# Optimization experiments

Hardware: AMD Instinct MI355X
Metric: run time of the kernel (lower is better)

## Reference

```python
import jax, jax.numpy as jnp
import numpy as np
from jax import lax

K = 9  # propagation kernel

def conv(x, w, b, pad):
    y = lax.conv_general_dilated(x, w, (1, 1), [(pad, pad), (pad, pad)],
                                 dimension_numbers=('NCHW', 'OIHW', 'NCHW'))
    return y + b[None, :, None, None]

def bn(x, g, beta):
    # SynchronizedBatchNorm2d in eval mode with identity running stats (mean=0, var=1)
    return x * g[None, :, None, None] + beta[None, :, None, None]

def propagate(deep, wts):
    # Dynamic local filtering (same math as img2col * weights, sum over 81 taps),
    # computed as 81 shifted-slice FMAs instead of materializing the (n,c,hw,81) tensor.
    p = K // 2
    n, c, h, w = deep.shape
    padded = jnp.pad(deep, ((0, 0), (0, 0), (p, p), (p, p)))
    out = jnp.zeros_like(deep)
    for k in range(K * K):  # k = dy*9 + dx, matching unfold(2).unfold(3) flattening
        dy, dx = k // K, k % K
        out = out + padded[:, :, dy:dy + h, dx:dx + w] * wts[:, k:k + 1]
    return out

def setup_inputs():
    key = jax.random.key(0)
    ks = jax.random.split(key, 40)
    N, C, H, W = 1, 256, 96, 192
    NUM_CLASSES = 19
    s = 0.05
    f32 = jnp.float32
    d = {}
    d['f1_deep'] = jax.random.normal(ks[0], (N, C, H, W), f32)
    d['f1_low'] = jax.random.normal(ks[1], (N, C, H, W), f32)
    d['f2_low'] = jax.random.normal(ks[2], (N, C, H, W), f32)
    # WeightPredictor
    d['wp_c1_w'] = jax.random.normal(ks[3], (256, 256, 3, 3), f32) * s
    d['wp_c1_b'] = jnp.zeros((256,), f32)
    d['wp_c2_w'] = jax.random.normal(ks[4], (256, 512, 3, 3), f32) * s
    d['wp_c2_b'] = jnp.zeros((256,), f32)
    d['wp_fc_w'] = jax.random.normal(ks[5], (81, 256, 1, 1), f32) * s
    d['wp_fc_b'] = jnp.zeros((81,), f32)
    # AdaptiveScheduler
    d['sch_c1_w'] = jax.random.normal(ks[6], (256, 256, 3, 3), f32) * s
    d['sch_c1_b'] = jnp.zeros((256,), f32)
    d['sch_c2_w'] = jax.random.normal(ks[7], (256, 256, 3, 3), f32) * s
    d['sch_c2_b'] = jnp.zeros((256,), f32)
    d['sch_fc_w'] = jax.random.normal(ks[8], (1, 256), f32) * s
    d['sch_fc_b'] = jnp.zeros((1,), f32)
    # AdaptNet
    d['ad_c1_w'] = jax.random.normal(ks[9], (256, 512, 3, 3), f32) * s
    d['ad_c1_b'] = jnp.zeros((256,), f32)
    d['ad_c2_w'] = jax.random.normal(ks[10], (256, 256, 3, 3), f32) * s
    d['ad_c2_b'] = jnp.zeros((256,), f32)
    d['ad_c3_w'] = jax.random.normal(ks[11], (256, 256, 3, 3), f32) * s
    d['ad_c3_b'] = jnp.zeros((256,), f32)
    # reduce_conv2 (1x1 conv + BN)
    d['rc_w'] = jax.random.normal(ks[12], (48, 256, 1, 1), f32) * s
    d['rc_b'] = jnp.zeros((48,), f32)
    d['rc_g'] = jnp.ones((48,), f32)
    d['rc_beta'] = jnp.zeros((48,), f32)
    # last_conv
    d['lc1_w'] = jax.random.normal(ks[13], (256, 304, 3, 3), f32) * s
    d['lc1_b'] = jnp.zeros((256,), f32)
    d['lc1_g'] = jnp.ones((256,), f32)
    d['lc1_beta'] = jnp.zeros((256,), f32)
    d['lc2_w'] = jax.random.normal(ks[14], (256, 256, 3, 3), f32) * s
    d['lc2_b'] = jnp.zeros((256,), f32)
    d['lc2_g'] = jnp.ones((256,), f32)
    d['lc2_beta'] = jnp.zeros((256,), f32)
    d['lc3_w'] = jax.random.normal(ks[15], (NUM_CLASSES, 256, 1, 1), f32) * s
    d['lc3_b'] = jnp.zeros((NUM_CLASSES,), f32)
    return d

def reference(f1_deep, f1_low, f2_low,
              wp_c1_w, wp_c1_b, wp_c2_w, wp_c2_b, wp_fc_w, wp_fc_b,
              sch_c1_w, sch_c1_b, sch_c2_w, sch_c2_b, sch_fc_w, sch_fc_b,
              ad_c1_w, ad_c1_b, ad_c2_w, ad_c2_b, ad_c3_w, ad_c3_b,
              rc_w, rc_b, rc_g, rc_beta,
              lc1_w, lc1_b, lc1_g, lc1_beta,
              lc2_w, lc2_b, lc2_g, lc2_beta,
              lc3_w, lc3_b):
    n, c, h, w = f1_deep.shape
    # WeightPredictor: shared conv1 applied to both low features, cat, conv2, 1x1, softmax over 81 taps
    a1 = conv(f1_low, wp_c1_w, wp_c1_b, 1)
    a2 = conv(f2_low, wp_c1_w, wp_c1_b, 1)
    f = conv(jnp.concatenate([a1, a2], axis=1), wp_c2_w, wp_c2_b, 1)
    kernel = jax.nn.softmax(conv(f, wp_fc_w, wp_fc_b, 0), axis=1)  # (n,81,h,w)
    # AdaptiveScheduler
    diff = conv(f1_low, sch_c1_w, sch_c1_b, 1) - conv(f2_low, sch_c1_w, sch_c1_b, 1)
    o = conv(diff, sch_c2_w, sch_c2_b, 1)
    pooled = jnp.mean(o, axis=(2, 3)).squeeze()  # (256,) since n=1
    deviation = pooled @ sch_fc_w.T + sch_fc_b  # (1,)
    # PropagationModule (dynamic 9x9 local filtering of f1_deep by predicted per-pixel kernel)
    prop = propagate(f1_deep, kernel)  # (n,256,h,w)
    # AdaptNet
    x = conv(jnp.concatenate([f2_low, prop], axis=1), ad_c1_w, ad_c1_b, 1)
    x = conv(x, ad_c2_w, ad_c2_b, 1)
    x = conv(x, ad_c3_w, ad_c3_b, 1)
    # reduce_conv2 + last_conv
    low = bn(conv(f2_low, rc_w, rc_b, 0), rc_g, rc_beta)  # (n,48,h,w)
    x = jnp.concatenate([x, low], axis=1)  # (n,304,h,w)
    x = bn(conv(x, lc1_w, lc1_b, 1), lc1_g, lc1_beta)
    x = bn(conv(x, lc2_w, lc2_b, 1), lc2_g, lc2_beta)
    x = conv(x, lc3_w, lc3_b, 0)  # (n,19,h,w)
    out = jax.image.resize(x, (x.shape[0], x.shape[1], 4 * h, 4 * w), method='bilinear')
    return (out, deviation)
```

## Files before the change

### kernel.cpp

```cpp
#include <hip/hip_runtime.h>
#include <math.h>

#define HWIMG 18432
#define W2 194
#define H2 98
#define NPX1 (H2 * W2)
#define W4 200
#define H4 104
#define NPX4 (H4 * W4)
#define NOUT (19 * 384 * 768)

typedef short bf16x8 __attribute__((ext_vector_type(8)));
typedef float f32x16 __attribute__((ext_vector_type(16)));

__device__ __forceinline__ ushort bf16r(float f) {
    union { float f; unsigned u; } a; a.f = f;
    unsigned u = a.u;
    return (ushort)((u + 0x7fffu + ((u >> 16) & 1u)) >> 16);
}
__device__ __forceinline__ float b2f(ushort u) {
    union { unsigned i; float f; } a; a.i = ((unsigned)u) << 16;
    return a.f;
}
__device__ __forceinline__ bf16x8 ld8(const ushort* p) {
    return *reinterpret_cast<const bf16x8*>(p);
}

__device__ __forceinline__ void gld16(const ushort* g, ushort* l) {
    __builtin_amdgcn_global_load_lds(
        (const __attribute__((address_space(1))) unsigned int*)g,
        (__attribute__((address_space(3))) unsigned int*)l, 16, 0, 0);
}

#define MF(a, b, c) __builtin_amdgcn_mfma_f32_32x32x16_bf16(a, b, c, 0, 0, 0)

__device__ __forceinline__ int swz(int L) { return L ^ (((L >> 7) & 7) << 4); }


__global__ __launch_bounds__(256) void xform_t_k(const float* __restrict__ src,
                                                 const float* __restrict__ src2,
                                                 ushort* __restrict__ dst)
{
    const int px = blockIdx.x * 32 + (threadIdx.x & 31);
    const int c8 = (blockIdx.y * 8 + (threadIdx.x >> 5)) * 8;
    if (px >= NPX1) return;
    const int yP = px / W2, xP = px % W2;
    const int y = yP - 1, x = xP - 1;
    ushort v[8];
    if (y >= 0 && y < 96 && x >= 0 && x < 192) {
        const int p = y * 192 + x;
#pragma unroll
        for (int j = 0; j < 8; ++j) {
            float f = src[(size_t)(c8 + j) * HWIMG + p];
            if (src2) f -= src2[(size_t)(c8 + j) * HWIMG + p];
            v[j] = bf16r(f);
        }
    } else {
#pragma unroll
        for (int j = 0; j < 8; ++j) v[j] = 0;
    }
    *reinterpret_cast<uint4*>(dst + ((size_t)(c8 >> 4) * NPX1 + px) * 16 + (c8 & 15))
        = *reinterpret_cast<uint4*>(v);
}

__global__ __launch_bounds__(256) void xform_nhwc_k(const float* __restrict__ src,
                                                    ushort* __restrict__ dst)
{
    const int px = blockIdx.x * 8 + (threadIdx.x >> 5);
    const int c8 = (threadIdx.x & 31) * 8;
    if (px >= NPX4) return;
    const int yP = px / W4, xP = px % W4;
    const int y = yP - 4, x = xP - 4;
    ushort v[8];
    if (y >= 0 && y < 96 && x >= 0 && x < 192) {
        const int p = y * 192 + x;
#pragma unroll
        for (int j = 0; j < 8; ++j) v[j] = bf16r(src[(size_t)(c8 + j) * HWIMG + p]);
    } else {
#pragma unroll
        for (int j = 0; j < 8; ++j) v[j] = 0;
    }
    *reinterpret_cast<uint4*>(dst + (size_t)px * 256 + c8) = *reinterpret_cast<uint4*>(v);
}

__global__ __launch_bounds__(256) void borderzero3_k(ushort* __restrict__ b0,
                                                     ushort* __restrict__ b1,
                                                     ushort* __restrict__ b2)
{
    ushort* buf = (blockIdx.y == 0) ? b0 : ((blockIdx.y == 1) ? b1 : b2);
    const int idx = blockIdx.x * 256 + threadIdx.x;
    if (idx >= 580 * 16) return;
    const int pi = idx % 580;
    const int cb = idx / 580;
    int pp;
    if (pi < 194) pp = pi;
    else if (pi < 388) pp = 97 * 194 + (pi - 194);
    else if (pi < 484) pp = (pi - 388 + 1) * 194;
    else pp = (pi - 484 + 1) * 194 + 193;
    uint4 z = {0, 0, 0, 0};
    ushort* p = buf + ((size_t)cb * NPX1 + pp) * 16;
    *reinterpret_cast<uint4*>(p) = z;
    *reinterpret_cast<uint4*>(p + 8) = z;
}

struct WtxJob {
    const float* w; const float* b; const float* g; const float* beta;
    int CoutR, Coutp, CinR0, kb0e, CinR1, KBt, ntaps, wtoff, biasoff;
};

__global__ __launch_bounds__(256) void wtx_multi_k(WtxJob J0, WtxJob J1, WtxJob J2,
                                                   WtxJob J3, WtxJob J4, WtxJob J5,
                                                   ushort* __restrict__ wt,
                                                   float* __restrict__ biasout)
{
    WtxJob J = J0;
    switch (blockIdx.y) {
        case 1: J = J1; break; case 2: J = J2; break; case 3: J = J3; break;
        case 4: J = J4; break; case 5: J = J5; break; default: break;
    }
    const int idx = blockIdx.x * 256 + threadIdx.x;
    const int total = J.ntaps * J.KBt * J.Coutp * 16;
    const int CinT = J.CinR0 + J.CinR1;
    if (idx < total) {
        const int c16 = idx & 15;
        const int oc = (idx >> 4) % J.Coutp;
        const int r2 = idx / (16 * J.Coutp);
        const int tap = r2 % J.ntaps;
        const int kbt = r2 / J.ntaps;
        const int k = kbt * 16 + c16;
        float val = 0.f;
        if (oc < J.CoutR) {
            int cit = -1;
            if (k < J.kb0e) { if (k < J.CinR0) cit = k; }
            else { const int k1 = k - J.kb0e; if (k1 < J.CinR1) cit = J.CinR0 + k1; }
            if (cit >= 0) {
                val = J.w[((size_t)oc * CinT + cit) * J.ntaps + tap];
                if (J.g) val *= J.g[oc];
            }
        }
        wt[J.wtoff + idx] = bf16r(val);
    } else if (idx < total + J.Coutp) {
        const int oc = idx - total;
        float v = 0.f;
        if (oc < J.CoutR) {
            v = J.b ? J.b[oc] : 0.f;
            if (J.g) v = v * J.g[oc] + J.beta[oc];
        }
        biasout[J.biasoff + oc] = v;
    }
}

struct ConvJob {
    const ushort* in0; const ushort* in1;
    int KB0, KB1;
    const ushort* wt;
    const float* bias;
    ushort* out;
    int CoutWr;
};

template<int NTAPS>
__global__ __launch_bounds__(128) void conv_lds_k(ConvJob j0, ConvJob j1, ConvJob j2,
                                                  int Coutp)
{
    constexpr int AROWS = (NTAPS == 9) ? 4 : 2;
    constexpr int AW = (NTAPS == 9) ? 66 : 64;
    constexpr int ASLOTS = AROWS * AW * 2;
    __shared__ __align__(128) ushort Abuf[AROWS * AW * 16];
    __shared__ __align__(128) ushort Bbuf[NTAPS * 64 * 16];

    ConvJob J = j0;
    if (blockIdx.y == 1) J = j1;
    else if (blockIdx.y == 2) J = j2;

    const int nblk = gridDim.x;
    const int cpx = nblk >> 3;
    const int sw = ((int)blockIdx.x & 7) * cpx + ((int)blockIdx.x >> 3);
    const int pt = sw % 144;
    const int ocb0 = (sw / 144) * 64;
    const int y0 = (pt / 3) * 2 + 1;
    const int x0 = (pt % 3) * 64 + 1;

    const int tid = threadIdx.x;
    const int lane = tid & 63;
    const int wm = tid >> 6;
    const int l31 = lane & 31;
    const int h16 = (lane >> 5) * 16;

    const int bl = swz(tid * 16);
    const int b_r = bl >> 5;
    const int b_h8 = ((bl >> 4) & 1) * 8;

    const int KBtot = J.KB0 + J.KB1;

    f32x16 c00 = {}, c01 = {}, c10 = {}, c11 = {};

    for (int kb = 0; kb < KBtot; ++kb) {
        const ushort* plane = (kb < J.KB0)
            ? (J.in0 + (size_t)kb * (NPX1 * 16))
            : (J.in1 + (size_t)(kb - J.KB0) * (NPX1 * 16));

#pragma unroll
        for (int i = 0; i < (ASLOTS + 127) / 128; ++i) {
            const int f16 = i * 128 + tid;
            if ((ASLOTS % 128 == 0) || (f16 < ASLOTS)) {
                const int L = swz(f16 * 16);
                const int e = L >> 5;
                const int h8 = ((L >> 4) & 1) * 8;
                const int r = e / AW;
                const int xx = e - r * AW;
                const int px = (NTAPS == 9)
                    ? (y0 - 1 + r) * W2 + (x0 - 1 + xx)
                    : (y0 + r) * W2 + (x0 + xx);
                const ushort* src = plane + (size_t)px * 16 + h8;
                const int wub = (f16 & ~63) * 16;
                gld16(src, (ushort*)((char*)Abuf + __builtin_amdgcn_readfirstlane(wub)));
            }
        }
        {
            const ushort* wsrc = J.wt + ((size_t)kb * NTAPS * Coutp + ocb0 + b_r) * 16 + b_h8;
#pragma unroll
            for (int t = 0; t < NTAPS; ++t) {
                const ushort* src = wsrc + (size_t)t * Coutp * 16;
                const int wub = t * 2048 + (tid & ~63) * 16;
                gld16(src, (ushort*)((char*)Bbuf + __builtin_amdgcn_readfirstlane(wub)));
            }
        }
        __syncthreads();

#pragma unroll
        for (int t = 0; t < NTAPS; ++t) {
            int entA;
            if (NTAPS == 9) entA = (wm + t / 3) * AW + (t % 3) + l31;
            else            entA = wm * 64 + l31;
            const int SA = swz(entA * 32 + h16);
            bf16x8 a0 = ld8((const ushort*)((const char*)Abuf + SA));
            bf16x8 a1 = ld8((const ushort*)((const char*)Abuf + SA + 1024));
            const int SB = swz((t * 64 + l31) * 32 + h16);
            bf16x8 b0 = ld8((const ushort*)((const char*)Bbuf + SB));
            bf16x8 b1 = ld8((const ushort*)((const char*)Bbuf + SB + 1024));
            c00 = MF(a0, b0, c00);
            c01 = MF(a0, b1, c01);
            c10 = MF(a1, b0, c10);
            c11 = MF(a1, b1, c11);
        }
        __syncthreads();
    }

    const int pxbase = (y0 + wm) * W2 + x0;
    const int rlo = (lane >> 5) * 4;
#pragma unroll
    for (int j = 0; j < 2; ++j) {
        if (ocb0 + j * 32 + 32 > J.CoutWr) continue;
        const int oc = ocb0 + j * 32 + l31;
        const float bs = J.bias[oc];
        const size_t obase = (size_t)(oc >> 4) * ((size_t)NPX1 * 16) + (oc & 15);
        const f32x16 v0 = j ? c01 : c00;
        const f32x16 v1 = j ? c11 : c10;
#pragma unroll
        for (int r = 0; r < 16; ++r) {
            const int rw = (r & 3) + 8 * (r >> 2) + rlo;
            J.out[obase + (size_t)(pxbase + rw) * 16] = bf16r(v0[r] + bs);
            J.out[obase + (size_t)(pxbase + 32 + rw) * 16] = bf16r(v1[r] + bs);
        }
    }
}

__global__ __launch_bounds__(256) void softmax81_k(ushort* __restrict__ t)
{
    const int p = blockIdx.x * 256 + threadIdx.x;
    if (p >= HWIMG) return;
    const int y = p / 192, x = p % 192;
    const size_t pp = (size_t)(y + 1) * W2 + (x + 1);
    float v[81];
    float m = -1e30f;
#pragma unroll
    for (int k = 0; k < 81; ++k) {
        v[k] = b2f(t[((size_t)(k >> 4) * NPX1 + pp) * 16 + (k & 15)]);
        m = fmaxf(m, v[k]);
    }
    float s = 0.f;
#pragma unroll
    for (int k = 0; k < 81; ++k) { v[k] = __expf(v[k] - m); s += v[k]; }
    const float inv = 1.f / s;
#pragma unroll
    for (int k = 0; k < 81; ++k)
        t[((size_t)(k >> 4) * NPX1 + pp) * 16 + (k & 15)] = bf16r(v[k] * inv);
}

__global__ __launch_bounds__(256) void prop_k(const ushort* __restrict__ deep,
                                              const ushort* __restrict__ ker,
                                              ushort* __restrict__ out)
{
    __shared__ float kl[8][81];
    const int pxb = blockIdx.x * 8;
    const int t = threadIdx.x;
    for (int i = t; i < 8 * 81; i += 256) {
        const int pp = pxb + i / 81, k = i % 81;
        float kv = 0.f;
        if (pp < NPX1) {
            const int yP = pp / W2, xP = pp % W2;
            if (yP >= 1 && yP <= 96 && xP >= 1 && xP <= 192)
                kv = b2f(ker[((size_t)(k >> 4) * NPX1 + pp) * 16 + (k & 15)]);
        }
        kl[i / 81][k] = kv;
    }
    __syncthreads();
    const int pi = t >> 5;
    const int c8 = (t & 31) * 8;
    const int pp = pxb + pi;
    if (pp >= NPX1) return;
    const int yP = pp / W2, xP = pp % W2;
    ushort* op = out + ((size_t)(c8 >> 4) * NPX1 + pp) * 16 + (c8 & 15);
    if (yP < 1 || yP > 96 || xP < 1 || xP > 192) {
        uint4 z = {0, 0, 0, 0};
        *reinterpret_cast<uint4*>(op) = z;
        return;
    }
    const int y = yP - 1, x = xP - 1;
    float acc[8];
#pragma unroll
    for (int j = 0; j < 8; ++j) acc[j] = 0.f;
    const ushort* dbase = deep + ((size_t)(y + 4) * W4 + (x + 4)) * 256 + c8;
#pragma unroll
    for (int k = 0; k < 81; ++k) {
        const int dy = k / 9 - 4, dx = k % 9 - 4;
        const float kv = kl[pi][k];
        bf16x8 d = ld8(dbase + (ptrdiff_t)(dy * W4 + dx) * 256);
#pragma unroll
        for (int j = 0; j < 8; ++j) acc[j] += b2f((ushort)d[j]) * kv;
    }
    ushort v[8];
#pragma unroll
    for (int j = 0; j < 8; ++j) v[j] = bf16r(acc[j]);
    *reinterpret_cast<uint4*>(op) = *reinterpret_cast<uint4*>(v);
}

__global__ __launch_bounds__(256) void rowsum_k(const ushort* __restrict__ t,
                                                float* __restrict__ partial)
{
    const int y = blockIdx.x, c = threadIdx.x;
    const size_t base = ((size_t)(c >> 4) * NPX1 + (size_t)(y + 1) * W2 + 1) * 16 + (c & 15);
    float s = 0.f;
    for (int x = 0; x < 192; ++x) s += b2f(t[base + (size_t)x * 16]);
    partial[y * 256 + c] = s;
}

__global__ __launch_bounds__(256) void dev_k(const float* __restrict__ partial,
                                             const float* __restrict__ fcw,
                                             const float* __restrict__ fcb,
                                             float* __restrict__ o)
{
    __shared__ float buf[256];
    const int c = threadIdx.x;
    float s = 0.f;
    for (int y = 0; y < 96; ++y) s += partial[y * 256 + c];
    buf[c] = s * fcw[c];
    __syncthreads();
    for (int st = 128; st > 0; st >>= 1) {
        if (c < st) buf[c] += buf[c + st];
        __syncthreads();
    }
    if (c == 0) o[0] = buf[0] * (1.f / (float)HWIMG) + fcb[0];
}

__global__ __launch_bounds__(256) void upsample_k(const ushort* __restrict__ in,
                                                  float* __restrict__ outp)
{
    const int idx = blockIdx.x * 256 + threadIdx.x;
    if (idx >= NOUT) return;
    const int ox = idx % 768;
    const int t = idx / 768;
    const int oy = t % 384;
    const int c = t / 384;

    const float fx = (ox + 0.5f) * 0.25f - 0.5f;
    const float fy = (oy + 0.5f) * 0.25f - 0.5f;
    const int x0 = (int)floorf(fx);
    const int y0 = (int)floorf(fy);
    const float wx = fx - (float)x0;
    const float wy = fy - (float)y0;
    const int x0c = min(max(x0, 0), 191), x1c = min(max(x0 + 1, 0), 191);
    const int y0c = min(max(y0, 0), 95), y1c = min(max(y0 + 1, 0), 95);

    const size_t cb = (size_t)(c >> 4) * NPX1;
    const int c16 = c & 15;
    const float v00 = b2f(in[(cb + (size_t)(y0c + 1) * W2 + (x0c + 1)) * 16 + c16]);
    const float v01 = b2f(in[(cb + (size_t)(y0c + 1) * W2 + (x1c + 1)) * 16 + c16]);
    const float v10 = b2f(in[(cb + (size_t)(y1c + 1) * W2 + (x0c + 1)) * 16 + c16]);
    const float v11 = b2f(in[(cb + (size_t)(y1c + 1) * W2 + (x1c + 1)) * 16 + c16]);
    outp[idx] = (1.f - wy) * ((1.f - wx) * v00 + wx * v01)
              + wy * ((1.f - wx) * v10 + wx * v11);
}

extern "C" void kernel_launch(void* const* d_in, const int* in_sizes, int n_in,
                              void* d_out, int out_size, void* d_ws, size_t ws_size,
                              hipStream_t stream)
{
    const float* f1_deep = (const float*)d_in[0];
    const float* f1_low  = (const float*)d_in[1];
    const float* f2_low  = (const float*)d_in[2];
    const float* wp_c1_w = (const float*)d_in[3];
    const float* wp_c1_b = (const float*)d_in[4];
    const float* wp_c2_w = (const float*)d_in[5];
    const float* wp_c2_b = (const float*)d_in[6];
    const float* wp_fc_w = (const float*)d_in[7];
    const float* wp_fc_b = (const float*)d_in[8];
    const float* sch_c1_w = (const float*)d_in[9];
    const float* sch_c2_w = (const float*)d_in[11];
    const float* sch_c2_b = (const float*)d_in[12];
    const float* sch_fc_w = (const float*)d_in[13];
    const float* sch_fc_b = (const float*)d_in[14];
    const float* ad_c1_w = (const float*)d_in[15];
    const float* ad_c1_b = (const float*)d_in[16];
    const float* ad_c2_w = (const float*)d_in[17];
    const float* ad_c2_b = (const float*)d_in[18];
    const float* ad_c3_w = (const float*)d_in[19];
    const float* ad_c3_b = (const float*)d_in[20];
    const float* rc_w    = (const float*)d_in[21];
    const float* rc_b    = (const float*)d_in[22];
    const float* rc_g    = (const float*)d_in[23];
    const float* rc_beta = (const float*)d_in[24];
    const float* lc1_w   = (const float*)d_in[25];
    const float* lc1_b   = (const float*)d_in[26];
    const float* lc1_g   = (const float*)d_in[27];
    const float* lc1_beta= (const float*)d_in[28];
    const float* lc2_w   = (const float*)d_in[29];
    const float* lc2_b   = (const float*)d_in[30];
    const float* lc2_g   = (const float*)d_in[31];
    const float* lc2_beta= (const float*)d_in[32];
    const float* lc3_w   = (const float*)d_in[33];
    const float* lc3_b   = (const float*)d_in[34];

    float* out = (float*)d_out;
    ushort* ws0 = (ushort*)d_ws;

    const size_t CBBe  = (size_t)NPX1 * 256;
    const size_t BUF0e = (size_t)NPX4 * 256;

    ushort* Bb = ws0 + BUF0e;
    ushort* Cb = Bb + CBBe;
    ushort* Db = Cb + CBBe;
    ushort* Eb = Db + CBBe;
    ushort* Fb = Eb + CBBe;
    ushort* WT = Fb + CBBe;
    float* BIAS = (float*)(WT + 3719168);
    float* PART = BIAS + 12 * 256;
    ushort* L48 = Eb + 6 * (size_t)NPX1 * 16;

    const dim3 b256(256), b128(128);

    xform_t_k<<<dim3(595, 4), b256, 0, stream>>>(f1_low, nullptr, Bb);
    xform_t_k<<<dim3(595, 4), b256, 0, stream>>>(f2_low, nullptr, Cb);
    xform_t_k<<<dim3(595, 4), b256, 0, stream>>>(f1_low, f2_low, Db);
    borderzero3_k<<<dim3(37, 3), b256, 0, stream>>>(ws0, Eb, Fb);

    {
        WtxJob w0 = {wp_c1_w, wp_c1_b, nullptr, nullptr, 256, 256, 256, 256, 0, 16, 9, 0, 0};
        WtxJob w1 = {sch_c1_w, nullptr, nullptr, nullptr, 256, 256, 256, 256, 0, 16, 9, 589824, 256};
        WtxJob w2 = {wp_c2_w, wp_c2_b, nullptr, nullptr, 256, 256, 256, 256, 256, 32, 9, 1179648, 512};
        WtxJob w3 = {sch_c2_w, sch_c2_b, nullptr, nullptr, 256, 256, 256, 256, 0, 16, 9, 2359296, 768};
        WtxJob w4 = {wp_fc_w, wp_fc_b, nullptr, nullptr, 81, 128, 256, 256, 0, 16, 1, 2949120, 1024};
        WtxJob w5 = {rc_w, rc_b, rc_g, rc_beta, 48, 128, 256, 256, 0, 16, 1, 2981888, 1280};
        wtx_multi_k<<<dim3(4610, 6), b256, 0, stream>>>(w0, w1, w2, w3, w4, w5, WT, BIAS);
    }

    {
        ConvJob a0 = {Bb, Bb, 16, 0, WT, BIAS, Eb, 256};
        ConvJob a1 = {Cb, Cb, 16, 0, WT, BIAS, Fb, 256};
        ConvJob a2 = {Db, Db, 16, 0, WT + 589824, BIAS + 256, ws0, 256};
        conv_lds_k<9><<<dim3(576, 3), b128, 0, stream>>>(a0, a1, a2, 256);
    }
    {
        ConvJob a0 = {Eb, Fb, 16, 16, WT + 1179648, BIAS + 512, Db, 256};
        ConvJob a1 = {ws0, ws0, 16, 0, WT + 2359296, BIAS + 768, Bb, 256};
        conv_lds_k<9><<<dim3(576, 2), b128, 0, stream>>>(a0, a1, a0, 256);
    }
    rowsum_k<<<96, b256, 0, stream>>>(Bb, PART);
    dev_k<<<1, b256, 0, stream>>>(PART, sch_fc_w, sch_fc_b, out + NOUT);

    {
        ConvJob a0 = {Db, Db, 16, 0, WT + 2949120, BIAS + 1024, Eb, 96};
        ConvJob a1 = {Cb, Cb, 16, 0, WT + 2981888, BIAS + 1280, L48, 64};
        conv_lds_k<1><<<dim3(288, 2), b128, 0, stream>>>(a0, a1, a0, 128);
    }

    {
        WtxJob w0 = {ad_c1_w, ad_c1_b, nullptr, nullptr, 256, 256, 256, 256, 256, 32, 9, 0, 1536};
        WtxJob w1 = {ad_c2_w, ad_c2_b, nullptr, nullptr, 256, 256, 256, 256, 0, 16, 9, 1179648, 1792};
        WtxJob w2 = {ad_c3_w, ad_c3_b, nullptr, nullptr, 256, 256, 256, 256, 0, 16, 9, 1769472, 2048};
        WtxJob w3 = {lc1_w, lc1_b, lc1_g, lc1_beta, 256, 256, 256, 256, 48, 20, 9, 2359296, 2304};
        WtxJob w4 = {lc2_w, lc2_b, lc2_g, lc2_beta, 256, 256, 256, 256, 0, 16, 9, 3096576, 2560};
        WtxJob w5 = {lc3_w, lc3_b, nullptr, nullptr, 19, 128, 256, 256, 0, 16, 1, 3686400, 2816};
        wtx_multi_k<<<dim3(4610, 6), b256, 0, stream>>>(w0, w1, w2, w3, w4, w5, WT, BIAS);
    }

    softmax81_k<<<72, b256, 0, stream>>>(Eb);
    xform_nhwc_k<<<2600, b256, 0, stream>>>(f1_deep, ws0);
    prop_k<<<2377, b256, 0, stream>>>(ws0, Eb, Fb);

    {
        ConvJob a = {Cb, Fb, 16, 16, WT, BIAS + 1536, Bb, 256};
        conv_lds_k<9><<<dim3(576, 1), b128, 0, stream>>>(a, a, a, 256);
    }
    {
        ConvJob a = {Bb, Bb, 16, 0, WT + 1179648, BIAS + 1792, Db, 256};
        conv_lds_k<9><<<dim3(576, 1), b128, 0, stream>>>(a, a, a, 256);
    }
    {
        ConvJob a = {Db, Db, 16, 0, WT + 1769472, BIAS + 2048, Fb, 256};
        conv_lds_k<9><<<dim3(576, 1), b128, 0, stream>>>(a, a, a, 256);
    }
    {
        ConvJob a = {Fb, L48, 16, 4, WT + 2359296, BIAS + 2304, Bb, 256};
        conv_lds_k<9><<<dim3(576, 1), b128, 0, stream>>>(a, a, a, 256);
    }
    {
        ConvJob a = {Bb, Bb, 16, 0, WT + 3096576, BIAS + 2560, Db, 256};
        conv_lds_k<9><<<dim3(576, 1), b128, 0, stream>>>(a, a, a, 256);
    }
    {
        ConvJob a = {Db, Db, 16, 0, WT + 3686400, BIAS + 2816, Cb, 32};
        conv_lds_k<1><<<dim3(288, 1), b128, 0, stream>>>(a, a, a, 128);
    }

    upsample_k<<<(NOUT + 255) / 256, b256, 0, stream>>>(Cb, out);
}
```

Before: 510.5 us.

## Double-buffer LDS staging in conv kernel and split rowsum across more blocks

The conv kernel now keeps two LDS buffers for the input and weight tiles. It issues the global-to-LDS loads for the next K-block before computing on the current one, which removes one barrier per iteration and overlaps memory with MFMA work. The rowsum reduction is split four ways per row, 384 blocks instead of 96, to raise parallelism, and the partial sums move to the start of the workspace (ws0). Doubling LDS use lowers occupancy. PART now sits on ws0, which conv_lds_k writes as the sch_c1 output and reads as the input to sch_c2; by the time rowsum runs that data has been consumed, but a later reader of that region would see it clobbered.

```diff
diff --git a/kernel.cpp b/kernel.cpp
--- a/kernel.cpp
+++ b/kernel.cpp
@@ -160,14 +160,50 @@
 };
 
 template<int NTAPS>
-__global__ __launch_bounds__(128) void conv_lds_k(ConvJob j0, ConvJob j1, ConvJob j2,
-                                                  int Coutp)
+__device__ __forceinline__ void stage_kb(
+    const ConvJob& J, int kb, char* Ab, char* Bb,
+    int y0, int x0, int ocb0, int Coutp, int tid, int b_r, int b_h8, int wu)
 {
     constexpr int AROWS = (NTAPS == 9) ? 4 : 2;
     constexpr int AW = (NTAPS == 9) ? 66 : 64;
     constexpr int ASLOTS = AROWS * AW * 2;
-    __shared__ __align__(128) ushort Abuf[AROWS * AW * 16];
-    __shared__ __align__(128) ushort Bbuf[NTAPS * 64 * 16];
+    const ushort* plane = (kb < J.KB0)
+        ? (J.in0 + (size_t)kb * (NPX1 * 16))
+        : (J.in1 + (size_t)(kb - J.KB0) * (NPX1 * 16));
+#pragma unroll
+    for (int i = 0; i < (ASLOTS + 127) / 128; ++i) {
+        const int f16 = i * 128 + tid;
+        if ((ASLOTS % 128 == 0) || (f16 < ASLOTS)) {
+            const int L = swz(f16 * 16);
+            const int e = L >> 5;
+            const int h8 = ((L >> 4) & 1) * 8;
+            const int r = e / AW;
+            const int xx = e - r * AW;
+            const int px = (NTAPS == 9)
+                ? (y0 - 1 + r) * W2 + (x0 - 1 + xx)
+                : (y0 + r) * W2 + (x0 + xx);
+            const ushort* src = plane + (size_t)px * 16 + h8;
+            const int wub = (f16 & ~63) * 16;
+            gld16(src, (ushort*)(Ab + __builtin_amdgcn_readfirstlane(wub)));
+        }
+    }
+    const ushort* wsrc = J.wt + ((size_t)kb * NTAPS * Coutp + ocb0 + b_r) * 16 + b_h8;
+#pragma unroll
+    for (int t = 0; t < NTAPS; ++t) {
+        gld16(wsrc + (size_t)t * Coutp * 16, (ushort*)(Bb + t * 2048 + wu));
+    }
+}
+
+template<int NTAPS>
+__global__ __launch_bounds__(128) void conv_lds_k(ConvJob j0, ConvJob j1, ConvJob j2,
+                                                  int Coutp)
+{
+    constexpr int AROWS = (NTAPS == 9) ? 4 : 2;
+    constexpr int AW = (NTAPS == 9) ? 66 : 64;
+    constexpr int ABYTES = AROWS * AW * 32;
+    constexpr int BBYTES = NTAPS * 64 * 32;
+    __shared__ __align__(128) char Abuf[2][ABYTES];
+    __shared__ __align__(128) char Bbuf[2][BBYTES];
 
     ConvJob J = j0;
     if (blockIdx.y == 1) J = j1;
@@ -190,61 +226,39 @@
     const int bl = swz(tid * 16);
     const int b_r = bl >> 5;
     const int b_h8 = ((bl >> 4) & 1) * 8;
+    const int wu = __builtin_amdgcn_readfirstlane((tid & ~63) * 16);
 
     const int KBtot = J.KB0 + J.KB1;
 
     f32x16 c00 = {}, c01 = {}, c10 = {}, c11 = {};
 
+    stage_kb<NTAPS>(J, 0, Abuf[0], Bbuf[0], y0, x0, ocb0, Coutp, tid, b_r, b_h8, wu);
+
+    int cur = 0;
     for (int kb = 0; kb < KBtot; ++kb) {
-        const ushort* plane = (kb < J.KB0)
-            ? (J.in0 + (size_t)kb * (NPX1 * 16))
-            : (J.in1 + (size_t)(kb - J.KB0) * (NPX1 * 16));
-
-#pragma unroll
-        for (int i = 0; i < (ASLOTS + 127) / 128; ++i) {
-            const int f16 = i * 128 + tid;
-            if ((ASLOTS % 128 == 0) || (f16 < ASLOTS)) {
-                const int L = swz(f16 * 16);
-                const int e = L >> 5;
-                const int h8 = ((L >> 4) & 1) * 8;
-                const int r = e / AW;
-                const int xx = e - r * AW;
-                const int px = (NTAPS == 9)
-                    ? (y0 - 1 + r) * W2 + (x0 - 1 + xx)
-                    : (y0 + r) * W2 + (x0 + xx);
-                const ushort* src = plane + (size_t)px * 16 + h8;
-                const int wub = (f16 & ~63) * 16;
-                gld16(src, (ushort*)((char*)Abuf + __builtin_amdgcn_readfirstlane(wub)));
-            }
-        }
-        {
-            const ushort* wsrc = J.wt + ((size_t)kb * NTAPS * Coutp + ocb0 + b_r) * 16 + b_h8;
-#pragma unroll
-            for (int t = 0; t < NTAPS; ++t) {
-                const ushort* src = wsrc + (size_t)t * Coutp * 16;
-                const int wub = t * 2048 + (tid & ~63) * 16;
-                gld16(src, (ushort*)((char*)Bbuf + __builtin_amdgcn_readfirstlane(wub)));
-            }
-        }
         __syncthreads();
-
+        if (kb + 1 < KBtot)
+            stage_kb<NTAPS>(J, kb + 1, Abuf[cur ^ 1], Bbuf[cur ^ 1],
+                            y0, x0, ocb0, Coutp, tid, b_r, b_h8, wu);
+        const char* Ab = Abuf[cur];
+        const char* Bb = Bbuf[cur];
 #pragma unroll
         for (int t = 0; t < NTAPS; ++t) {
             int entA;
             if (NTAPS == 9) entA = (wm + t / 3) * AW + (t % 3) + l31;
             else            entA = wm * 64 + l31;
             const int SA = swz(entA * 32 + h16);
-            bf16x8 a0 = ld8((const ushort*)((const char*)Abuf + SA));
-            bf16x8 a1 = ld8((const ushort*)((const char*)Abuf + SA + 1024));
+            bf16x8 a0 = ld8((const ushort*)(Ab + SA));
+            bf16x8 a1 = ld8((const ushort*)(Ab + SA + 1024));
             const int SB = swz((t * 64 + l31) * 32 + h16);
-            bf16x8 b0 = ld8((const ushort*)((const char*)Bbuf + SB));
-            bf16x8 b1 = ld8((const ushort*)((const char*)Bbuf + SB + 1024));
+            bf16x8 b0 = ld8((const ushort*)(Bb + SB));
+            bf16x8 b1 = ld8((const ushort*)(Bb + SB + 1024));
             c00 = MF(a0, b0, c00);
             c01 = MF(a0, b1, c01);
             c10 = MF(a1, b0, c10);
             c11 = MF(a1, b1, c11);
         }
-        __syncthreads();
+        cur ^= 1;
     }
 
     const int pxbase = (y0 + wm) * W2 + x0;
@@ -339,11 +353,14 @@
 __global__ __launch_bounds__(256) void rowsum_k(const ushort* __restrict__ t,
                                                 float* __restrict__ partial)
 {
-    const int y = blockIdx.x, c = threadIdx.x;
-    const size_t base = ((size_t)(c >> 4) * NPX1 + (size_t)(y + 1) * W2 + 1) * 16 + (c & 15);
+    const int y = blockIdx.x >> 2;
+    const int bx = blockIdx.x & 3;
+    const int c = threadIdx.x;
+    const size_t base = ((size_t)(c >> 4) * NPX1 + (size_t)(y + 1) * W2 + 1 + bx * 48) * 16
+                      + (c & 15);
     float s = 0.f;
-    for (int x = 0; x < 192; ++x) s += b2f(t[base + (size_t)x * 16]);
-    partial[y * 256 + c] = s;
+    for (int x = 0; x < 48; ++x) s += b2f(t[base + (size_t)x * 16]);
+    partial[(size_t)blockIdx.x * 256 + c] = s;
 }
 
 __global__ __launch_bounds__(256) void dev_k(const float* __restrict__ partial,
@@ -354,7 +371,7 @@
     __shared__ float buf[256];
     const int c = threadIdx.x;
     float s = 0.f;
-    for (int y = 0; y < 96; ++y) s += partial[y * 256 + c];
+    for (int i = 0; i < 384; ++i) s += partial[(size_t)i * 256 + c];
     buf[c] = s * fcw[c];
     __syncthreads();
     for (int st = 128; st > 0; st >>= 1) {
@@ -445,7 +462,7 @@
     ushort* Fb = Eb + CBBe;
     ushort* WT = Fb + CBBe;
     float* BIAS = (float*)(WT + 3719168);
-    float* PART = BIAS + 12 * 256;
+    float* PART = (float*)ws0;
     ushort* L48 = Eb + 6 * (size_t)NPX1 * 16;
 
     const dim3 b256(256), b128(128);
@@ -476,7 +493,7 @@
         ConvJob a1 = {ws0, ws0, 16, 0, WT + 2359296, BIAS + 768, Bb, 256};
         conv_lds_k<9><<<dim3(576, 2), b128, 0, stream>>>(a0, a1, a0, 256);
     }
-    rowsum_k<<<96, b256, 0, stream>>>(Bb, PART);
+    rowsum_k<<<384, b256, 0, stream>>>(Bb, PART);
     dev_k<<<1, b256, 0, stream>>>(PART, sch_fc_w, sch_fc_b, out + NOUT);
 
     {
```

Measured after the change: 515.4 us. About the same (+1.0%).
